# Kernel optimization log

Hardware: AMD Instinct MI355X
Metric: run time of the kernel (lower is better)

The kernel has to match this reference:

```python
import jax, jax.numpy as jnp
import numpy as np
from jax import lax

B = 32768
N_INP = 256
N_HIDDEN = 1024
N_F = 256
N_ITERS = 100  # fixed-point solver iteration count in Convex


def _make_operators(n_f):
    # D = tridiag(-1, 2, -1) with first/last rows zeroed; mid = 0.5 * (sub+super diag ones)
    D = (-np.diag(np.ones(n_f - 1), -1) + 2 * np.diag(np.ones(n_f))
         - np.diag(np.ones(n_f - 1), 1)).astype(np.float32)
    D[0, :] = 0.0
    D[n_f - 1, :] = 0.0
    mid = 0.5 * (np.diag(np.ones(n_f - 1), -1) + np.diag(np.ones(n_f - 1), 1)).astype(np.float32)
    return jnp.asarray(D), jnp.asarray(mid)


def _convex(param):
    # param: [B, n_f]  (the torch code carries [B, n_f, 1]; column vec is equivalent)
    D, mid = _make_operators(param.shape[-1])

    def body(z, _):
        zx = z + param                       # [B, n_f]
        Dz = jnp.einsum('ij,bj->bi', D, zx)  # D @ zx
        mz = jnp.einsum('ij,bj->bi', mid, zx)
        dx = jnp.where(Dz > 0, zx - mz, 0.0)
        return zx - dx - param, None

    z0 = jnp.zeros_like(param)
    z_star, _ = lax.scan(body, z0, None, length=N_ITERS)
    return param + z_star  # Convex.forward: x + model(x)


def setup_inputs() -> dict:
    key = jax.random.key(0)
    k = jax.random.split(key, 5)
    x = jax.random.uniform(k[0], (B, N_INP + 1), dtype=jnp.float32)
    W1 = jax.random.normal(k[1], (N_HIDDEN, N_INP), dtype=jnp.float32) * 0.02
    b1 = jax.random.normal(k[2], (N_HIDDEN,), dtype=jnp.float32) * 0.02
    W2 = jax.random.normal(k[3], (N_F, N_HIDDEN), dtype=jnp.float32) * 0.02
    b2 = jax.random.normal(k[4], (N_F,), dtype=jnp.float32) * 0.02
    return {"x": x, "W1": W1, "b1": b1, "W2": W2, "b2": b2}


def reference(x, W1, b1, W2, b2):
    h = jax.nn.relu(x[..., :N_INP] @ W1.T + b1)     # [B, n_hidden]
    x_ = h @ W2.T + b2                              # [B, n_f]
    param = _convex(x_)                             # [B, n_f]
    # EvalConvex: round(query * (n_f - 1)) -> gather along feature dim
    idx = jnp.round(x[..., N_INP] * (N_F - 1)).astype(jnp.int32)  # [B]
    out = jnp.take_along_axis(param, idx[:, None], axis=1)        # [B, 1]
    return out.reshape(-1, 1, 1)                                  # [B, 1, 1]
```

## Files before the change

### kernel.cpp

```cpp
#include <hip/hip_runtime.h>
#include <stdint.h>

#define B_ROWS 32768
#define N_INP 256
#define N_HID 1024
#define NF 256
#define N_IT 100

typedef __attribute__((ext_vector_type(8))) _Float16 f16x8;
typedef __attribute__((ext_vector_type(4))) float f32x4;
typedef __attribute__((ext_vector_type(2))) _Float16 f16x2;
typedef uint32_t u32;

__device__ __forceinline__ ushort f2h(float f) {
  _Float16 h = (_Float16)f;
  return *reinterpret_cast<ushort*>(&h);
}

__device__ __forceinline__ void async_copy16(const void* g, void* l) {
  __builtin_amdgcn_global_load_lds(
      (const __attribute__((address_space(1))) void*)g,
      (__attribute__((address_space(3))) void*)l, 16, 0, 0);
}

__device__ __forceinline__ f16x2 as_h2(u32 x) { return __builtin_bit_cast(f16x2, x); }
__device__ __forceinline__ u32 as_u32(f16x2 x) { return __builtin_bit_cast(u32, x); }
__device__ __forceinline__ f16x2 min2(f16x2 a, f16x2 b) {
  f16x2 r;
  asm("v_pk_min_f16 %0, %1, %2" : "=v"(r) : "v"(a), "v"(b));
  return r;
}

__global__ void prep_kernel(const float* __restrict__ x,
                            const float* __restrict__ W1,
                            const float* __restrict__ W2,
                            ushort* __restrict__ xh,
                            ushort* __restrict__ w1h,
                            ushort* __restrict__ w2h,
                            int* __restrict__ idx) {
  if (blockIdx.x < 8192) {
    int t = blockIdx.x * 256 + threadIdx.x;
    int b = t >> 6, q = t & 63;
    const float* xr = x + (size_t)b * (N_INP + 1);
    float v0 = xr[q * 4 + 0], v1 = xr[q * 4 + 1], v2 = xr[q * 4 + 2], v3 = xr[q * 4 + 3];
    ushort4 u = make_ushort4(f2h(v0), f2h(v1), f2h(v2), f2h(v3));
    *reinterpret_cast<ushort4*>(xh + (size_t)b * 256 + q * 4) = u;
    if (q == 0) idx[b] = (int)rintf(xr[N_INP] * 255.0f);
  } else {
    int t = (blockIdx.x - 8192) * 256 + threadIdx.x;
    float4 a = reinterpret_cast<const float4*>(W1)[t];
    float4 b = reinterpret_cast<const float4*>(W2)[t];
    reinterpret_cast<ushort4*>(w1h)[t] = make_ushort4(f2h(a.x), f2h(a.y), f2h(a.z), f2h(a.w));
    reinterpret_cast<ushort4*>(w2h)[t] = make_ushort4(f2h(b.x), f2h(b.y), f2h(b.z), f2h(b.w));
  }
}

template <int RELU>
__global__ __launch_bounds__(256, 2) void gemm_bt(
    const ushort* __restrict__ A, const ushort* __restrict__ Bw,
    const float* __restrict__ bias, ushort* __restrict__ C,
    int M, int N, int K, int ntN) {
  __shared__ ushort As[2][128 * 64];
  __shared__ ushort Bs[2][128 * 64];
  const int tid = threadIdx.x;
  const int w = tid >> 6, l = tid & 63;
  int bid = blockIdx.x;
  if (((int)gridDim.x & 7) == 0) {
    int cpx = (int)gridDim.x >> 3;
    bid = (bid & 7) * cpx + (bid >> 3);
  }
  const int tm = bid / ntN, tn = bid % ntN;
  const int wm = w >> 1, wn = w & 1;
  const char* Ab = (const char*)(A + (size_t)tm * 128 * K);
  const char* Bb = (const char*)(Bw + (size_t)tn * 128 * K);
  const int sA = K * 2;
  const int lrow = l >> 3;
  const int lcol = (l & 7) * 16;

  f32x4 acc[4][4];
#pragma unroll
  for (int i = 0; i < 4; ++i)
#pragma unroll
    for (int j = 0; j < 4; ++j) acc[i][j] = {0.f, 0.f, 0.f, 0.f};

  const int nkt = K / 64;
  {
    const char* ga = Ab + lrow * sA + lcol;
    const char* gb = Bb + lrow * sA + lcol;
#pragma unroll
    for (int i = 0; i < 4; ++i) {
      int c = w * 4 + i;
      async_copy16(ga + c * 8 * sA, (char*)&As[0][0] + c * 1024);
      async_copy16(gb + c * 8 * sA, (char*)&Bs[0][0] + c * 1024);
    }
  }
  __syncthreads();

  const int arow = wm * 64 + (l & 15);
  const int brow = wn * 64 + (l & 15);
  const int koff = (l >> 4) * 8;

  for (int kt = 0; kt < nkt; ++kt) {
    const int buf = kt & 1;
    if (kt + 1 < nkt) {
      const char* ga = Ab + (kt + 1) * 128 + lrow * sA + lcol;
      const char* gb = Bb + (kt + 1) * 128 + lrow * sA + lcol;
#pragma unroll
      for (int i = 0; i < 4; ++i) {
        int c = w * 4 + i;
        async_copy16(ga + c * 8 * sA, (char*)&As[buf ^ 1][0] + c * 1024);
        async_copy16(gb + c * 8 * sA, (char*)&Bs[buf ^ 1][0] + c * 1024);
      }
    }
#pragma unroll
    for (int ks = 0; ks < 2; ++ks) {
      f16x8 af[4], bfr[4];
#pragma unroll
      for (int mi = 0; mi < 4; ++mi)
        af[mi] = *(const f16x8*)&As[buf][(arow + mi * 16) * 64 + ks * 32 + koff];
#pragma unroll
      for (int ni = 0; ni < 4; ++ni)
        bfr[ni] = *(const f16x8*)&Bs[buf][(brow + ni * 16) * 64 + ks * 32 + koff];
#pragma unroll
      for (int mi = 0; mi < 4; ++mi)
#pragma unroll
        for (int ni = 0; ni < 4; ++ni)
          acc[mi][ni] = __builtin_amdgcn_mfma_f32_16x16x32_f16(
              af[mi], bfr[ni], acc[mi][ni], 0, 0, 0);
    }
    __syncthreads();
  }

  const int grow0 = tm * 128 + wm * 64 + (l >> 4) * 4;
  const int gcol0 = tn * 128 + wn * 64 + (l & 15);
#pragma unroll
  for (int ni = 0; ni < 4; ++ni) {
    const int col = gcol0 + ni * 16;
    const float bv = bias[col];
#pragma unroll
    for (int mi = 0; mi < 4; ++mi) {
      const int row = grow0 + mi * 16;
#pragma unroll
      for (int r = 0; r < 4; ++r) {
        float v = acc[mi][ni][r] + bv;
        if (RELU) v = fmaxf(v, 0.f);
        C[(size_t)(row + r) * N + col] = f2h(v);
      }
    }
  }
}

__global__ __launch_bounds__(1024, 8) void gemm2_convex(
    const ushort* __restrict__ A,
    const ushort* __restrict__ Bw,
    const float* __restrict__ bias,
    const int* __restrict__ idxp,
    float* __restrict__ out) {
  __shared__ ushort smem[20480];
  const int tid = threadIdx.x;
  const int w = tid >> 6, l = tid & 63;
  const int wm = w >> 2, wn = w & 3;
  const int m0r = blockIdx.x * 64;

  f32x4 acc[4];
#pragma unroll
  for (int i = 0; i < 4; ++i) acc[i] = {0.f, 0.f, 0.f, 0.f};

  const int srow = tid >> 2;
  const int scs = (tid & 3) ^ ((srow >> 1) & 3);
  const ushort* gA = A + (size_t)(m0r + srow) * N_HID + scs * 8;
  const ushort* gB = Bw + (size_t)srow * N_HID + scs * 8;

#define STAGE(kt, buf)                                                  \
  {                                                                     \
    if (tid < 256) async_copy16(gA + (kt) * 32, smem + (buf) * 2048 + tid * 8); \
    async_copy16(gB + (kt) * 32, smem + 4096 + (buf) * 8192 + tid * 8); \
  }

  STAGE(0, 0);
  __syncthreads();

  const int arow = wm * 16 + (l & 15);
  const int brow0 = wn * 64 + (l & 15);
  const int kx = (((l >> 4) ^ ((l >> 1) & 3)) * 8);

  for (int kt = 0; kt < 32; ++kt) {
    const int buf = kt & 1;
    if (kt < 31) STAGE(kt + 1, buf ^ 1);
    f16x8 af = *(const f16x8*)(smem + buf * 2048 + arow * 32 + kx);
#pragma unroll
    for (int ni = 0; ni < 4; ++ni) {
      f16x8 bf = *(const f16x8*)(smem + 4096 + buf * 8192 + (brow0 + ni * 16) * 32 + kx);
      acc[ni] = __builtin_amdgcn_mfma_f32_16x16x32_f16(af, bf, acc[ni], 0, 0, 0);
    }
    __syncthreads();
  }
#undef STAGE

  {
    const int r0 = wm * 16 + (l >> 4) * 4;
    const int c0 = wn * 64 + (l & 15);
#pragma unroll
    for (int ni = 0; ni < 4; ++ni) {
      const int col = c0 + ni * 16;
      const float bv = bias[col];
#pragma unroll
      for (int r = 0; r < 4; ++r)
        smem[(r0 + r) * 256 + col] = f2h(acc[ni][r] + bv);
    }
  }
  __syncthreads();

  const int q = l & 15;
  const int row = w * 4 + (l >> 4);
  u32 w0, w1, w2, w3, w4, w5, w6, w7;
  {
    const uint4* src = reinterpret_cast<const uint4*>(smem + row * 256 + q * 16);
    uint4 v0 = src[0], v1 = src[1];
    w0 = v0.x; w1 = v0.y; w2 = v0.z; w3 = v0.w;
    w4 = v1.x; w5 = v1.y; w6 = v1.z; w7 = v1.w;
  }
  const int ii = idxp[m0r + row];
  const int upIdx = ((l - 1) & 63) * 4;
  const int dnIdx = ((l + 1) & 63) * 4;
  const bool fixP = (q == 0);
  const bool fixN = (q == 15);
  const f16x2 halfc = {(_Float16)0.5f, (_Float16)0.5f};

  u32 P = __builtin_amdgcn_ds_bpermute(upIdx, w7);
  u32 N = __builtin_amdgcn_ds_bpermute(dnIdx, w0);

#define AB(hi, lo) as_h2(__builtin_amdgcn_alignbit((hi), (lo), 16))
#define UPD(wj, sa, sb) wj = as_u32(min2(as_h2(wj), ((sa) + (sb)) * halfc))
#pragma unroll 2
  for (int it = 0; it < N_IT; ++it) {
    const u32 Pf = fixP ? 0x7C000000u : P;
    const u32 Nf = fixN ? 0x00007C00u : N;
    f16x2 s0 = AB(w0, Pf), s1 = AB(w1, w0), s2 = AB(w2, w1), s3 = AB(w3, w2);
    f16x2 s4 = AB(w4, w3), s5 = AB(w5, w4), s6 = AB(w6, w5), s7 = AB(w7, w6);
    f16x2 s8 = AB(Nf, w7);
    UPD(w7, s7, s8);
    UPD(w0, s0, s1);
    P = __builtin_amdgcn_ds_bpermute(upIdx, w7);
    N = __builtin_amdgcn_ds_bpermute(dnIdx, w0);
    UPD(w1, s1, s2); UPD(w2, s2, s3); UPD(w3, s3, s4);
    UPD(w4, s4, s5); UPD(w5, s5, s6); UPD(w6, s6, s7);
  }
#undef AB
#undef UPD

  const int sel = (ii >> 1) & 7;
  u32 a0 = (sel & 4) ? w4 : w0, a1 = (sel & 4) ? w5 : w1;
  u32 a2 = (sel & 4) ? w6 : w2, a3 = (sel & 4) ? w7 : w3;
  u32 b0 = (sel & 2) ? a2 : a0, b1 = (sel & 2) ? a3 : a1;
  u32 c0 = (sel & 1) ? b1 : b0;
  ushort hv = (ii & 1) ? (ushort)(c0 >> 16) : (ushort)(c0 & 0xffffu);
  float v = (float)__builtin_bit_cast(_Float16, hv);
  v = __shfl(v, (l & ~15) | (ii >> 4));
  if (q == 0) out[m0r + row] = v;
}

extern "C" void kernel_launch(void* const* d_in, const int* in_sizes, int n_in,
                              void* d_out, int out_size, void* d_ws, size_t ws_size,
                              hipStream_t stream) {
  const float* x = (const float*)d_in[0];
  const float* W1 = (const float*)d_in[1];
  const float* b1 = (const float*)d_in[2];
  const float* W2 = (const float*)d_in[3];
  const float* b2 = (const float*)d_in[4];
  float* out = (float*)d_out;

  char* ws = (char*)d_ws;
  ushort* xh  = (ushort*)ws;
  ushort* w1h = (ushort*)(ws + 16777216);
  ushort* w2h = (ushort*)(ws + 17301504);
  int*    idx = (int*)  (ws + 17825792);
  ushort* h   = (ushort*)(ws + 17956864);

  const size_t fixed = 17956864;
  int chunk = 2048;
  if (ws_size >= fixed + (size_t)32768 * 2048) chunk = 32768;
  else if (ws_size >= fixed + (size_t)16384 * 2048) chunk = 16384;
  else if (ws_size >= fixed + (size_t)8192 * 2048) chunk = 8192;
  else if (ws_size >= fixed + (size_t)4096 * 2048) chunk = 4096;

  prep_kernel<<<8448, 256, 0, stream>>>(x, W1, W2, xh, w1h, w2h, idx);

  for (int m0 = 0; m0 < B_ROWS; m0 += chunk) {
    int curM = (B_ROWS - m0 < chunk) ? (B_ROWS - m0) : chunk;
    dim3 g1((curM / 128) * (N_HID / 128));
    gemm_bt<1><<<g1, 256, 0, stream>>>(xh + (size_t)m0 * 256, w1h, b1, h,
                                       curM, N_HID, N_INP, N_HID / 128);
    gemm2_convex<<<curM / 64, 1024, 0, stream>>>(h, w2h, b2, idx + m0, out + m0);
  }
}
```

Baseline: 125.4 us.

## Fuse fp32-to-fp16 conversion of x into first GEMM's A-tile staging

```diff
diff --git a/kernel.cpp b/kernel.cpp
--- a/kernel.cpp
+++ b/kernel.cpp
@@ -10,11 +10,18 @@
 typedef __attribute__((ext_vector_type(8))) _Float16 f16x8;
 typedef __attribute__((ext_vector_type(4))) float f32x4;
 typedef __attribute__((ext_vector_type(2))) _Float16 f16x2;
+typedef float f32x4a __attribute__((ext_vector_type(4), aligned(4)));
 typedef uint32_t u32;
 
 __device__ __forceinline__ ushort f2h(float f) {
   _Float16 h = (_Float16)f;
   return *reinterpret_cast<ushort*>(&h);
+}
+
+__device__ __forceinline__ u32 pkh(float a, float b) {
+  _Float16 ha = (_Float16)a, hb = (_Float16)b;
+  return (u32)*reinterpret_cast<ushort*>(&ha) |
+         ((u32)*reinterpret_cast<ushort*>(&hb) << 16);
 }
 
 __device__ __forceinline__ void async_copy16(const void* g, void* l) {
@@ -34,36 +41,31 @@
 __global__ void prep_kernel(const float* __restrict__ x,
                             const float* __restrict__ W1,
                             const float* __restrict__ W2,
-                            ushort* __restrict__ xh,
                             ushort* __restrict__ w1h,
                             ushort* __restrict__ w2h,
                             int* __restrict__ idx) {
-  if (blockIdx.x < 8192) {
+  if (blockIdx.x < 256) {
     int t = blockIdx.x * 256 + threadIdx.x;
-    int b = t >> 6, q = t & 63;
-    const float* xr = x + (size_t)b * (N_INP + 1);
-    float v0 = xr[q * 4 + 0], v1 = xr[q * 4 + 1], v2 = xr[q * 4 + 2], v3 = xr[q * 4 + 3];
-    ushort4 u = make_ushort4(f2h(v0), f2h(v1), f2h(v2), f2h(v3));
-    *reinterpret_cast<ushort4*>(xh + (size_t)b * 256 + q * 4) = u;
-    if (q == 0) idx[b] = (int)rintf(xr[N_INP] * 255.0f);
-  } else {
-    int t = (blockIdx.x - 8192) * 256 + threadIdx.x;
     float4 a = reinterpret_cast<const float4*>(W1)[t];
     float4 b = reinterpret_cast<const float4*>(W2)[t];
     reinterpret_cast<ushort4*>(w1h)[t] = make_ushort4(f2h(a.x), f2h(a.y), f2h(a.z), f2h(a.w));
     reinterpret_cast<ushort4*>(w2h)[t] = make_ushort4(f2h(b.x), f2h(b.y), f2h(b.z), f2h(b.w));
-  }
-}
-
-template <int RELU>
-__global__ __launch_bounds__(256, 2) void gemm_bt(
-    const ushort* __restrict__ A, const ushort* __restrict__ Bw,
-    const float* __restrict__ bias, ushort* __restrict__ C,
-    int M, int N, int K, int ntN) {
+  } else {
+    int r = (blockIdx.x - 256) * 256 + threadIdx.x;
+    idx[r] = (int)rintf(x[(size_t)r * 257 + 256] * 255.0f);
+  }
+}
+
+__global__ __launch_bounds__(256) void gemm1_x(
+    const float* __restrict__ X,
+    const ushort* __restrict__ Bw,
+    const float* __restrict__ bias,
+    ushort* __restrict__ C,
+    int ntN) {
   __shared__ ushort As[2][128 * 64];
   __shared__ ushort Bs[2][128 * 64];
-  const int tid = threadIdx.x;
-  const int w = tid >> 6, l = tid & 63;
+  const int t = threadIdx.x;
+  const int w = t >> 6, l = t & 63;
   int bid = blockIdx.x;
   if (((int)gridDim.x & 7) == 0) {
     int cpx = (int)gridDim.x >> 3;
@@ -71,46 +73,69 @@
   }
   const int tm = bid / ntN, tn = bid % ntN;
   const int wm = w >> 1, wn = w & 1;
-  const char* Ab = (const char*)(A + (size_t)tm * 128 * K);
-  const char* Bb = (const char*)(Bw + (size_t)tn * 128 * K);
-  const int sA = K * 2;
+
+  const float* Xb = X + (size_t)(tm * 128) * 257;
+  const char* Bb = (const char*)(Bw + (size_t)tn * 128 * 256);
+  const int sB = 512;
   const int lrow = l >> 3;
   const int lcol = (l & 7) * 16;
 
+  const int ar0 = t >> 3;
+  const int ak0 = (t & 7) * 8;
+
+  f32x4a a0, a1, a2, a3, a4, a5, a6, a7;
+#define LOADA(kt)                                                        \
+  {                                                                      \
+    const float* p0 = Xb + (size_t)ar0 * 257 + (kt) * 64 + ak0;          \
+    const float* p1 = p0 + (size_t)32 * 257;                             \
+    const float* p2 = p0 + (size_t)64 * 257;                             \
+    const float* p3 = p0 + (size_t)96 * 257;                             \
+    a0 = *(const f32x4a*)p0; a1 = *(const f32x4a*)(p0 + 4);              \
+    a2 = *(const f32x4a*)p1; a3 = *(const f32x4a*)(p1 + 4);              \
+    a4 = *(const f32x4a*)p2; a5 = *(const f32x4a*)(p2 + 4);              \
+    a6 = *(const f32x4a*)p3; a7 = *(const f32x4a*)(p3 + 4);              \
+  }
+#define WRITEA(buf)                                                      \
+  {                                                                      \
+    uint4* d = (uint4*)((char*)&As[buf][0] + t * 16);                    \
+    d[0]   = make_uint4(pkh(a0.x, a0.y), pkh(a0.z, a0.w),                \
+                        pkh(a1.x, a1.y), pkh(a1.z, a1.w));               \
+    d[256] = make_uint4(pkh(a2.x, a2.y), pkh(a2.z, a2.w),                \
+                        pkh(a3.x, a3.y), pkh(a3.z, a3.w));               \
+    d[512] = make_uint4(pkh(a4.x, a4.y), pkh(a4.z, a4.w),                \
+                        pkh(a5.x, a5.y), pkh(a5.z, a5.w));               \
+    d[768] = make_uint4(pkh(a6.x, a6.y), pkh(a6.z, a6.w),                \
+                        pkh(a7.x, a7.y), pkh(a7.z, a7.w));               \
+  }
+#define STAGEB(kt, buf)                                                  \
+  {                                                                      \
+    const char* gb = Bb + lrow * sB + (kt) * 128 + lcol;                 \
+    _Pragma("unroll") for (int i = 0; i < 4; ++i) {                      \
+      int c = w * 4 + i;                                                 \
+      async_copy16(gb + c * 8 * sB, (char*)&Bs[buf][0] + c * 1024);      \
+    }                                                                    \
+  }
+
   f32x4 acc[4][4];
 #pragma unroll
   for (int i = 0; i < 4; ++i)
 #pragma unroll
     for (int j = 0; j < 4; ++j) acc[i][j] = {0.f, 0.f, 0.f, 0.f};
 
-  const int nkt = K / 64;
-  {
-    const char* ga = Ab + lrow * sA + lcol;
-    const char* gb = Bb + lrow * sA + lcol;
-#pragma unroll
-    for (int i = 0; i < 4; ++i) {
-      int c = w * 4 + i;
-      async_copy16(ga + c * 8 * sA, (char*)&As[0][0] + c * 1024);
-      async_copy16(gb + c * 8 * sA, (char*)&Bs[0][0] + c * 1024);
-    }
-  }
+  LOADA(0);
+  STAGEB(0, 0);
+  WRITEA(0);
   __syncthreads();
 
   const int arow = wm * 64 + (l & 15);
   const int brow = wn * 64 + (l & 15);
   const int koff = (l >> 4) * 8;
 
-  for (int kt = 0; kt < nkt; ++kt) {
+  for (int kt = 0; kt < 4; ++kt) {
     const int buf = kt & 1;
-    if (kt + 1 < nkt) {
-      const char* ga = Ab + (kt + 1) * 128 + lrow * sA + lcol;
-      const char* gb = Bb + (kt + 1) * 128 + lrow * sA + lcol;
-#pragma unroll
-      for (int i = 0; i < 4; ++i) {
-        int c = w * 4 + i;
-        async_copy16(ga + c * 8 * sA, (char*)&As[buf ^ 1][0] + c * 1024);
-        async_copy16(gb + c * 8 * sA, (char*)&Bs[buf ^ 1][0] + c * 1024);
-      }
+    if (kt < 3) {
+      LOADA(kt + 1);
+      STAGEB(kt + 1, buf ^ 1);
     }
 #pragma unroll
     for (int ks = 0; ks < 2; ++ks) {
@@ -128,8 +153,12 @@
           acc[mi][ni] = __builtin_amdgcn_mfma_f32_16x16x32_f16(
               af[mi], bfr[ni], acc[mi][ni], 0, 0, 0);
     }
+    if (kt < 3) WRITEA(buf ^ 1);
     __syncthreads();
   }
+#undef LOADA
+#undef WRITEA
+#undef STAGEB
 
   const int grow0 = tm * 128 + wm * 64 + (l >> 4) * 4;
   const int gcol0 = tn * 128 + wn * 64 + (l & 15);
@@ -142,9 +171,8 @@
       const int row = grow0 + mi * 16;
 #pragma unroll
       for (int r = 0; r < 4; ++r) {
-        float v = acc[mi][ni][r] + bv;
-        if (RELU) v = fmaxf(v, 0.f);
-        C[(size_t)(row + r) * N + col] = f2h(v);
+        float v = fmaxf(acc[mi][ni][r] + bv, 0.f);
+        C[(size_t)(row + r) * N_HID + col] = f2h(v);
       }
     }
   }
@@ -271,26 +299,25 @@
   float* out = (float*)d_out;
 
   char* ws = (char*)d_ws;
-  ushort* xh  = (ushort*)ws;
-  ushort* w1h = (ushort*)(ws + 16777216);
-  ushort* w2h = (ushort*)(ws + 17301504);
-  int*    idx = (int*)  (ws + 17825792);
-  ushort* h   = (ushort*)(ws + 17956864);
-
-  const size_t fixed = 17956864;
+  ushort* w1h = (ushort*)ws;
+  ushort* w2h = (ushort*)(ws + 524288);
+  int*    idx = (int*)  (ws + 1048576);
+  ushort* h   = (ushort*)(ws + 1179648);
+
+  const size_t fixed = 1179648;
   int chunk = 2048;
   if (ws_size >= fixed + (size_t)32768 * 2048) chunk = 32768;
   else if (ws_size >= fixed + (size_t)16384 * 2048) chunk = 16384;
   else if (ws_size >= fixed + (size_t)8192 * 2048) chunk = 8192;
   else if (ws_size >= fixed + (size_t)4096 * 2048) chunk = 4096;
 
-  prep_kernel<<<8448, 256, 0, stream>>>(x, W1, W2, xh, w1h, w2h, idx);
+  prep_kernel<<<384, 256, 0, stream>>>(x, W1, W2, w1h, w2h, idx);
 
   for (int m0 = 0; m0 < B_ROWS; m0 += chunk) {
     int curM = (B_ROWS - m0 < chunk) ? (B_ROWS - m0) : chunk;
     dim3 g1((curM / 128) * (N_HID / 128));
-    gemm_bt<1><<<g1, 256, 0, stream>>>(xh + (size_t)m0 * 256, w1h, b1, h,
-                                       curM, N_HID, N_INP, N_HID / 128);
+    gemm1_x<<<g1, 256, 0, stream>>>(x + (size_t)m0 * 257, w1h, b1, h,
+                                    N_HID / 128);
     gemm2_convex<<<curM / 64, 1024, 0, stream>>>(h, w2h, b2, idx + m0, out + m0);
   }
 }
```

After: 122.5 us. -2.3%, faster.
